# Optimization experiments

Measured on AMD Instinct MI355X. Metric: run time of the kernel, lower is better.

## Reference

```python
import jax, jax.numpy as jnp
import numpy as np

B_SZ, SEQ_LEN, STATE_DIM, D_IN, D_OUT, KX = 8, 2048, 1024, 512, 512, 10


def setup_inputs() -> dict:
    key = jax.random.key(0)
    ks = jax.random.split(key, 7)
    inputs = jax.random.normal(ks[0], (B_SZ, SEQ_LEN, D_IN), dtype=jnp.float32)
    h0 = jax.random.normal(ks[1], (STATE_DIM,), dtype=jnp.float32)
    # exponential_decay_init(lam=15): x = clamp(-1/lam * log(1-u), max=1); A = (1-x)*sign
    u = jax.random.uniform(ks[2], (STATE_DIM,), dtype=jnp.float32)
    x = jnp.minimum(-(1.0 / 15.0) * jnp.log1p(-u), 1.0)
    sign = jnp.sign(jax.random.normal(ks[3], (STATE_DIM,), dtype=jnp.float32))
    A = (1.0 - x) * sign
    Bm = jax.random.normal(ks[4], (D_IN, STATE_DIM), dtype=jnp.float32) / D_IN
    C = jax.random.normal(ks[5], (STATE_DIM, D_OUT), dtype=jnp.float32) / STATE_DIM
    M = jax.random.normal(ks[6], (D_OUT, D_IN, KX), dtype=jnp.float32) / D_OUT
    return {"inputs": inputs, "h0": h0, "A": A, "B": Bm, "C": C, "M": M}


def _ar_preds(M, x):
    # Equivalent to einsum('oik,bli->bklo') + per-k roll + triu mask + sum over k:
    # ar[b,l,:] = sum_{i=0}^{k-1, i<=l} M[:,:,i] @ x[b, l-i, :]
    b, l, d_in = x.shape
    kx = M.shape[2]
    ar = jnp.einsum('oi,bli->blo', M[:, :, 0], x)
    for i in range(1, kx):
        x_shift = jnp.pad(x, ((0, 0), (i, 0), (0, 0)))[:, :l]  # shift right, zero-fill
        ar = ar + jnp.einsum('oi,bli->blo', M[:, :, i], x_shift)
    return ar


def reference(inputs, h0, A, B, C, M):
    b, l, d_in = inputs.shape
    state_dim = A.shape[0]
    # Project inputs once: u_t @ B for all t -> [b, l, s]
    uB = jnp.einsum('bli,is->bls', inputs, B)

    def step(h, u_t):
        h = A * h + u_t  # diagonal recurrence
        return h, h

    h_init = jnp.broadcast_to(h0, (b, state_dim))
    _, hs = jax.lax.scan(step, h_init, jnp.swapaxes(uB, 0, 1))  # [l, b, s]
    hs = jnp.swapaxes(hs, 0, 1)  # [b, l, s]
    lds_out = hs @ C  # [b, l, d_out]
    return lds_out + _ar_preds(M, inputs)
```

## Files before the change

### kernel.cpp

```cpp
#include <hip/hip_runtime.h>

#define B_SZ   8
#define SEQ    2048
#define PSEQ   (SEQ+16)
#define SDIM   1024
#define DIN    512
#define DOUT   512
#define KX     10
#define RTOT   (B_SZ*SEQ)
#define LC     64
#define NC     (SEQ/LC)

typedef __attribute__((ext_vector_type(8))) short short8;
typedef __attribute__((ext_vector_type(4))) float f32x4;
typedef __attribute__((ext_vector_type(4))) unsigned short bfx4;

#define OFF_XP   0UL
#define OFF_UB   16973824UL
#define OFF_HS   50528256UL
#define OFF_BT   84082688UL
#define OFF_CT   85131264UL
#define OFF_MT   86179840UL

__device__ __forceinline__ short f2bf(float f) {
  unsigned u = __builtin_bit_cast(unsigned, f);
  u += 0x7fffu + ((u >> 16) & 1u);
  return (short)(u >> 16);
}
__device__ __forceinline__ float bf2f(unsigned short b) {
  return __builtin_bit_cast(float, (unsigned)b << 16);
}

#define GLOAD16(gp, lp) __builtin_amdgcn_global_load_lds( \
    (const __attribute__((address_space(1))) void*)(gp), \
    (__attribute__((address_space(3))) void*)(lp), 16, 0, 0)
#define WAITVM(n) asm volatile("s_waitcnt vmcnt(" #n ")" ::: "memory")
#define LGKM0()   do { asm volatile("s_waitcnt lgkmcnt(0)" ::: "memory"); \
                       __builtin_amdgcn_sched_barrier(0); } while (0)
#define SBAR() __builtin_amdgcn_s_barrier()

__device__ __forceinline__ void transpose_tile(const float* __restrict__ in,
                                               short* __restrict__ out,
                                               int rows, int cols, int bxi, int byi,
                                               int tid, float (*t)[33]) {
  int bx = bxi * 32, by = byi * 32;
  int tx = tid & 31, ty = tid >> 5;
  #pragma unroll
  for (int j = 0; j < 32; j += 8)
    t[ty + j][tx] = in[(size_t)(by + ty + j) * cols + (bx + tx)];
  __syncthreads();
  #pragma unroll
  for (int j = 0; j < 32; j += 8)
    out[(size_t)(bx + ty + j) * rows + (by + tx)] = f2bf(t[tx][ty + j]);
}

__global__ void k_prep(const float* __restrict__ x,  const float* __restrict__ B,
                       const float* __restrict__ C,  const float* __restrict__ M,
                       short* __restrict__ Xp, short* __restrict__ Bt,
                       short* __restrict__ Ct, short* __restrict__ Mt) {
  __shared__ float t[32][33];
  int blk = blockIdx.x, tid = threadIdx.x;
  if (blk < 2048) {
    const int NG = RTOT * (DIN / 8);
    const int NPAD = B_SZ * 16 * (DIN / 8);
    for (int g = blk * 256 + tid; g < NG + NPAD; g += 2048 * 256) {
      if (g < NG) {
        int r = g >> 6, c8 = g & 63;
        int b = r >> 11, tt = r & 2047;
        const float4* p = reinterpret_cast<const float4*>(x) + (size_t)g * 2;
        float4 f0 = p[0], f1 = p[1];
        short8 o;
        o[0]=f2bf(f0.x); o[1]=f2bf(f0.y); o[2]=f2bf(f0.z); o[3]=f2bf(f0.w);
        o[4]=f2bf(f1.x); o[5]=f2bf(f1.y); o[6]=f2bf(f1.z); o[7]=f2bf(f1.w);
        *reinterpret_cast<short8*>(Xp + ((size_t)(b * PSEQ + 16 + tt) * DIN + c8 * 8)) = o;
      } else {
        int idx = g - NG;
        int b = idx >> 10, rem = idx & 1023;
        int row16 = rem >> 6, c8 = rem & 63;
        const short8 z = {0,0,0,0,0,0,0,0};
        *reinterpret_cast<short8*>(Xp + ((size_t)(b * PSEQ + row16) * DIN + c8 * 8)) = z;
      }
    }
  } else if (blk < 2560) {
    int idx = blk - 2048;
    transpose_tile(B, Bt, DIN, SDIM, idx & 31, idx >> 5, tid, t);
  } else if (blk < 3072) {
    int idx = blk - 2560;
    transpose_tile(C, Ct, SDIM, DOUT, idx & 15, idx >> 4, tid, t);
  } else {
    int idx = (blk - 3072) * 256 + tid;
    if (idx < DOUT * DIN) {
      int o = idx / DIN, i = idx - o * DIN;
      const float* src = M + ((size_t)o * DIN + i) * KX;
      #pragma unroll
      for (int tt = 0; tt < KX; ++tt)
        Mt[((size_t)tt * DOUT + o) * DIN + i] = f2bf(src[tt]);
    }
  }
}

__global__ void k_scan_E(const short* __restrict__ uB, const float* __restrict__ A,
                         float* __restrict__ E) {
  int blk = blockIdx.x, tid = threadIdx.x;
  int b = blk >> 5, c = blk & 31;
  int s0 = tid * 4;
  const short* base = uB + ((size_t)b * SEQ + (size_t)c * LC) * SDIM + s0;
  float a[4], h[4];
  #pragma unroll
  for (int j = 0; j < 4; ++j) { a[j] = A[s0 + j]; h[j] = 0.f; }
  for (int t = 0; t < LC; ++t) {
    bfx4 v = *reinterpret_cast<const bfx4*>(base + (size_t)t * SDIM);
    #pragma unroll
    for (int j = 0; j < 4; ++j) h[j] = fmaf(a[j], h[j], bf2f(v[j]));
  }
  float* ep = E + (size_t)blk * SDIM + s0;
  #pragma unroll
  for (int j = 0; j < 4; ++j) ep[j] = h[j];
}

__global__ void k_scan_h(const short* __restrict__ uB, const float* __restrict__ A,
                         const float* __restrict__ h0, const float* __restrict__ E,
                         short* __restrict__ hs) {
  int blk = blockIdx.x, tid = threadIdx.x;
  int b = blk >> 5, c = blk & 31;
  int s0 = tid * 4;
  float a[4], h[4], ap[4];
  #pragma unroll
  for (int j = 0; j < 4; ++j) {
    a[j] = A[s0 + j];
    float p = a[j];
    #pragma unroll
    for (int q = 0; q < 6; ++q) p *= p;
    ap[j] = p;
    h[j] = h0[s0 + j];
  }
  const float* Eb = E + (size_t)b * NC * SDIM + s0;
  for (int c2 = 0; c2 < c; ++c2) {
    float4 ev = *reinterpret_cast<const float4*>(Eb + (size_t)c2 * SDIM);
    h[0] = fmaf(ap[0], h[0], ev.x);
    h[1] = fmaf(ap[1], h[1], ev.y);
    h[2] = fmaf(ap[2], h[2], ev.z);
    h[3] = fmaf(ap[3], h[3], ev.w);
  }
  const short* base = uB + ((size_t)b * SEQ + (size_t)c * LC) * SDIM + s0;
  short* hbase = hs + ((size_t)b * SEQ + (size_t)c * LC) * SDIM + s0;
  for (int t = 0; t < LC; ++t) {
    bfx4 v = *reinterpret_cast<const bfx4*>(base + (size_t)t * SDIM);
    bfx4 o;
    #pragma unroll
    for (int j = 0; j < 4; ++j) {
      h[j] = fmaf(a[j], h[j], bf2f(v[j]));
      o[j] = (unsigned short)f2bf(h[j]);
    }
    *reinterpret_cast<bfx4*>(hbase + (size_t)t * SDIM) = o;
  }
}

__device__ __forceinline__ void stage128(const short* __restrict__ g, int ld,
                                         short* l, int tid) {
  int rsub = tid >> 3;
  int slot = (tid & 7) ^ (rsub & 7);
  #pragma unroll
  for (int i = 0; i < 4; ++i) {
    int row = i * 32 + rsub;
    GLOAD16(g + (size_t)row * ld + slot * 8, l + row * 64 + (tid & 7) * 8);
  }
}

__device__ __forceinline__ void mfma_tile(const short* lA, int aoff, const short* lB,
                                          int lane, int wm, int wn, f32x4 acc[4][4]) {
  int lr = lane & 15;
  int h  = lane >> 4;
  #pragma unroll
  for (int kk = 0; kk < 2; ++kk) {
    int kslot = kk * 4 + h;
    short8 af[4], bfr[4];
    #pragma unroll
    for (int mi = 0; mi < 4; ++mi) {
      int row = aoff + wm * 64 + mi * 16 + lr;
      af[mi] = *reinterpret_cast<const short8*>(lA + row * 64 + ((kslot ^ (row & 7)) << 3));
    }
    #pragma unroll
    for (int ni = 0; ni < 4; ++ni) {
      int row = wn * 64 + ni * 16 + lr;
      bfr[ni] = *reinterpret_cast<const short8*>(lB + row * 64 + ((kslot ^ (row & 7)) << 3));
    }
    __builtin_amdgcn_s_setprio(1);
    #pragma unroll
    for (int mi = 0; mi < 4; ++mi)
      #pragma unroll
      for (int ni = 0; ni < 4; ++ni)
        acc[mi][ni] = __builtin_amdgcn_mfma_f32_16x16x32_bf16(af[mi], bfr[ni], acc[mi][ni], 0, 0, 0);
    __builtin_amdgcn_s_setprio(0);
  }
}

__global__ __launch_bounds__(256) void k_gemm_uB(const short* __restrict__ Xp,
                                                 const short* __restrict__ Bt,
                                                 short* __restrict__ uB) {
  __shared__ __attribute__((aligned(16))) short lds[32768];
  short* A0 = lds;         short* B0 = lds + 8192;
  short* A1 = lds + 16384; short* B1 = lds + 24576;
  int tid = threadIdx.x, lane = tid & 63, w = tid >> 6, wm = w >> 1, wn = w & 1;
  long r0 = (long)blockIdx.x * 128;
  int  c0 = blockIdx.y * 128;
  int  b  = (int)(r0 >> 11);
  const short* Abase = Xp + (size_t)(r0 + 16 * (b + 1)) * DIN;
  const short* Bbase = Bt + (size_t)c0 * DIN;
  const f32x4 z4 = {0.f, 0.f, 0.f, 0.f};
  f32x4 acc[4][4];
  #pragma unroll
  for (int mi = 0; mi < 4; ++mi)
    #pragma unroll
    for (int ni = 0; ni < 4; ++ni) acc[mi][ni] = z4;

  stage128(Abase, DIN, A0, tid);      stage128(Bbase, DIN, B0, tid);
  stage128(Abase + 64, DIN, A1, tid); stage128(Bbase + 64, DIN, B1, tid);
  WAITVM(8);
  SBAR();
  for (int kt = 0; kt < 8; ++kt) {
    const short* a  = (kt & 1) ? A1 : A0;
    const short* bb = (kt & 1) ? B1 : B0;
    mfma_tile(a, 0, bb, lane, wm, wn, acc);
    SBAR();
    if (kt + 2 < 8) {
      short* ad = (kt & 1) ? A1 : A0;
      short* bd = (kt & 1) ? B1 : B0;
      stage128(Abase + (kt + 2) * 64, DIN, ad, tid);
      stage128(Bbase + (kt + 2) * 64, DIN, bd, tid);
      WAITVM(8);
    } else {
      WAITVM(0);
    }
    SBAR();
  }
  #pragma unroll
  for (int mi = 0; mi < 4; ++mi)
    #pragma unroll
    for (int ni = 0; ni < 4; ++ni)
      #pragma unroll
      for (int r = 0; r < 4; ++r) {
        long row = r0 + wm * 64 + mi * 16 + (lane >> 4) * 4 + r;
        int  col = c0 + wn * 64 + ni * 16 + (lane & 15);
        uB[(size_t)row * SDIM + col] = f2bf(acc[mi][ni][r]);
      }
}

struct Frags { short8 a[4][2]; short8 b[4][2]; };

__device__ __forceinline__ void read_frags(Frags& f, const short* la, int aoff,
                                           const short* lb, int lane, int wm, int wn) {
  int lr = lane & 15, h = lane >> 4;
  #pragma unroll
  for (int kk = 0; kk < 2; ++kk) {
    int kslot = kk * 4 + h;
    #pragma unroll
    for (int mi = 0; mi < 4; ++mi) {
      int row = aoff + wm * 64 + mi * 16 + lr;
      f.a[mi][kk] = *reinterpret_cast<const short8*>(la + row * 64 + ((kslot ^ (row & 7)) << 3));
    }
    #pragma unroll
    for (int ni = 0; ni < 4; ++ni) {
      int row = wn * 64 + ni * 16 + lr;
      f.b[ni][kk] = *reinterpret_cast<const short8*>(lb + row * 64 + ((kslot ^ (row & 7)) << 3));
    }
  }
}

__device__ __forceinline__ void mfma_frags(const Frags& f, f32x4 acc[4][4]) {
  #pragma unroll
  for (int kk = 0; kk < 2; ++kk)
    #pragma unroll
    for (int mi = 0; mi < 4; ++mi)
      #pragma unroll
      for (int ni = 0; ni < 4; ++ni)
        acc[mi][ni] = __builtin_amdgcn_mfma_f32_16x16x32_bf16(f.a[mi][kk], f.b[ni][kk], acc[mi][ni], 0, 0, 0);
}

__device__ __forceinline__ void sgb_interleave() {
  #pragma unroll
  for (int i = 0; i < 16; ++i) {
    __builtin_amdgcn_sched_group_barrier(0x008, 2, 0);
    __builtin_amdgcn_sched_group_barrier(0x100, 1, 0);
  }
}

__device__ __forceinline__ void stageA256(const short* __restrict__ g, int ld,
                                          short* l, int tid) {
  int rsub = tid >> 3;
  int slot = (tid & 7) ^ (rsub & 7);
  #pragma unroll
  for (int i = 0; i < 4; ++i) {
    int row = i * 64 + rsub;
    GLOAD16(g + (size_t)row * ld + slot * 8, l + row * 64 + (tid & 7) * 8);
  }
}
__device__ __forceinline__ void stageB128(const short* __restrict__ g, int ld,
                                          short* l, int tid) {
  int rsub = tid >> 3;
  int slot = (tid & 7) ^ (rsub & 7);
  #pragma unroll
  for (int i = 0; i < 2; ++i) {
    int row = i * 64 + rsub;
    GLOAD16(g + (size_t)row * ld + slot * 8, l + row * 64 + (tid & 7) * 8);
  }
}
__device__ __forceinline__ void stageX320(const short* __restrict__ g,
                                          short* l, int tid) {
  int rsub = tid >> 3;
  int slot = (tid & 7) ^ (rsub & 7);
  #pragma unroll
  for (int i = 0; i < 5; ++i) {
    int row = i * 64 + rsub;
    GLOAD16(g + (size_t)row * DIN + slot * 8, l + row * 64 + (tid & 7) * 8);
  }
}

__global__ __launch_bounds__(512, 2) void k_gemm_out(const short* __restrict__ hs,
                                                     const short* __restrict__ Xp,
                                                     const short* __restrict__ Ct,
                                                     const short* __restrict__ Mt,
                                                     float* __restrict__ out) {
  __shared__ __attribute__((aligned(16))) short lds[81920];
  short* const P0  = lds;
  short* const P1  = lds + 24576;
  short* const P2  = lds + 49152;
  short* const Xs0 = lds;
  short* const Xs1 = lds + 20480;
  short* const PM0 = lds + 57344;
  short* const PM1 = lds + 65536;
  short* const PM2 = lds + 73728;
  int tid = threadIdx.x, lane = tid & 63, w = tid >> 6;
  int wm = w >> 1, wn = w & 1;
  int bid = blockIdx.x;
  int sw  = (bid & 7) * 32 + (bid >> 3);
  long r0 = (long)(sw & 63) * 256;
  int  c0 = (sw >> 6) * 128;
  int  b  = (int)(r0 >> 11);
  const short* hsA = hs + (size_t)r0 * SDIM;
  const short* CtB = Ct + (size_t)c0 * SDIM;
  const short* Xa  = Xp + (size_t)(r0 + 16 * (b + 1) - 16) * DIN;
  const short* MtB = Mt + (size_t)c0 * DIN;

  const f32x4 z4 = {0.f, 0.f, 0.f, 0.f};
  f32x4 acc[4][4];
  #pragma unroll
  for (int mi = 0; mi < 4; ++mi)
    #pragma unroll
    for (int ni = 0; ni < 4; ++ni) acc[mi][ni] = z4;

  Frags fr[2];

  stageA256(hsA,        SDIM, P0, tid);  stageB128(CtB,        SDIM, P0 + 16384, tid);
  stageA256(hsA + 64,   SDIM, P1, tid);  stageB128(CtB + 64,   SDIM, P1 + 16384, tid);
  stageA256(hsA + 128,  SDIM, P2, tid);  stageB128(CtB + 128,  SDIM, P2 + 16384, tid);
  WAITVM(6);
  SBAR();
  read_frags(fr[0], P0, 0, P0 + 16384, lane, wm, wn);

  #pragma unroll
  for (int s = 0; s < 16; ++s) {
    __builtin_amdgcn_s_setprio(1);
    mfma_frags(fr[s & 1], acc);
    if (s < 15) {
      const short* nb = ((s + 1) % 3 == 0) ? P0 : ((s + 1) % 3 == 1) ? P1 : P2;
      read_frags(fr[(s + 1) & 1], nb, 0, nb + 16384, lane, wm, wn);
    } else {
      read_frags(fr[0], Xs0, 16, PM0, lane, wm, wn);
    }
    sgb_interleave();
    __builtin_amdgcn_s_setprio(0);
    LGKM0();
    SBAR();
    if (s <= 12) {
      short* sp = (s % 3 == 0) ? P0 : (s % 3 == 1) ? P1 : P2;
      stageA256(hsA + (s + 3) * 64, SDIM, sp, tid);
      stageB128(CtB + (s + 3) * 64, SDIM, sp + 16384, tid);
      WAITVM(6);
    } else if (s == 13) {
      stageB128(MtB, DIN, PM0, tid);
      stageB128(MtB + (size_t)DOUT * DIN, DIN, PM1, tid);
      WAITVM(4);
    } else if (s == 14) {
      stageB128(MtB + (size_t)2 * DOUT * DIN, DIN, PM2, tid);
      stageX320(Xa, Xs0, tid);
      WAITVM(0);
    }
    SBAR();
  }

  for (int k0 = 0; k0 < 8; ++k0) {
    int kc = k0 * 64;
    const short* xs = (k0 & 1) ? Xs1 : Xs0;
    short*       xn = (k0 & 1) ? Xs0 : Xs1;
    const short* q0 = (k0 % 3 == 0) ? PM0 : (k0 % 3 == 1) ? PM1 : PM2;
    const short* q1 = (k0 % 3 == 0) ? PM1 : (k0 % 3 == 1) ? PM2 : PM0;
    const short* q2 = (k0 % 3 == 0) ? PM2 : (k0 % 3 == 1) ? PM0 : PM1;
    #pragma unroll
    for (int j = 0; j < KX; ++j) {
      __builtin_amdgcn_s_setprio(1);
      mfma_frags(fr[j & 1], acc);
      bool do_read = (j < 9) || (k0 < 7);
      if (j < 9) {
        const short* mn = ((j + 1) % 3 == 0) ? q0 : ((j + 1) % 3 == 1) ? q1 : q2;
        read_frags(fr[(j + 1) & 1], xs, 15 - j, mn, lane, wm, wn);
      } else if (k0 < 7) {
        read_frags(fr[0], xn, 16, q1, lane, wm, wn);
      }
      if (do_read) sgb_interleave();
      __builtin_amdgcn_s_setprio(0);
      LGKM0();
      SBAR();
      if (j + 3 <= 9) {
        short* mw = (j % 3 == 0) ? (short*)q0 : (j % 3 == 1) ? (short*)q1 : (short*)q2;
        stageB128(MtB + (size_t)(j + 3) * DOUT * DIN + kc, DIN, mw, tid);
      } else if (k0 < 7) {
        short* mw = (j % 3 == 0) ? (short*)q0 : (j % 3 == 1) ? (short*)q1 : (short*)q2;
        stageB128(MtB + (size_t)(j - 7) * DOUT * DIN + kc + 64, DIN, mw, tid);
      }
      if (j == 1 && k0 < 7) stageX320(Xa + kc + 64, xn, tid);
      if (j == 1 || j == 2) {
        if (k0 < 7) { WAITVM(7); } else { WAITVM(2); }
      } else if (j >= 7) {
        if (k0 == 7) { WAITVM(0); } else { WAITVM(2); }
      } else {
        WAITVM(2);
      }
      SBAR();
    }
  }

  #pragma unroll
  for (int mi = 0; mi < 4; ++mi)
    #pragma unroll
    for (int ni = 0; ni < 4; ++ni)
      #pragma unroll
      for (int r = 0; r < 4; ++r) {
        long row = r0 + wm * 64 + mi * 16 + (lane >> 4) * 4 + r;
        int  col = c0 + wn * 64 + ni * 16 + (lane & 15);
        out[(size_t)row * DOUT + col] = acc[mi][ni][r];
      }
}

extern "C" void kernel_launch(void* const* d_in, const int* in_sizes, int n_in,
                              void* d_out, int out_size, void* d_ws, size_t ws_size,
                              hipStream_t stream) {
  (void)in_sizes; (void)n_in; (void)out_size; (void)ws_size;
  const float* x  = (const float*)d_in[0];
  const float* h0 = (const float*)d_in[1];
  const float* A  = (const float*)d_in[2];
  const float* B  = (const float*)d_in[3];
  const float* C  = (const float*)d_in[4];
  const float* M  = (const float*)d_in[5];
  float* out = (float*)d_out;
  char* ws = (char*)d_ws;

  short* Xp  = (short*)(ws + OFF_XP);
  short* uB  = (short*)(ws + OFF_UB);
  short* hsb = (short*)(ws + OFF_HS);
  short* Bt  = (short*)(ws + OFF_BT);
  short* Ct  = (short*)(ws + OFF_CT);
  short* Mt  = (short*)(ws + OFF_MT);
  float* E   = out;

  k_prep<<<4096, 256, 0, stream>>>(x, B, C, M, Xp, Bt, Ct, Mt);
  k_gemm_uB<<<dim3(RTOT / 128, SDIM / 128), 256, 0, stream>>>(Xp, Bt, uB);
  k_scan_E<<<B_SZ * NC, 256, 0, stream>>>(uB, A, E);
  k_scan_h<<<B_SZ * NC, 256, 0, stream>>>(uB, A, h0, E, hsb);
  k_gemm_out<<<256, 512, 0, stream>>>(hsb, Xp, Ct, Mt, out);
}
```

Baseline: 151.8 us.

## Fuse chunk-end scan into uB GEMM epilogue and move C/M prep into scan kernel

The separate k_scan_E pass, which reread uB to compute each 64-step chunk's end state, is removed. The uB GEMM epilogue now computes that end state directly from its fp32 accumulators with powers of A and cross-lane shuffles. The C and M transpose/convert blocks move from the prep kernel into the k_scan_h launch so they run alongside the scan blocks. This saves one kernel launch and a full read of uB, at the cost of a heavier GEMM epilogue and a slight numeric difference, since E is now built from fp32 accumulators rather than bf16-rounded uB.

```diff
diff --git a/kernel.cpp b/kernel.cpp
--- a/kernel.cpp
+++ b/kernel.cpp
@@ -39,25 +39,8 @@
                        __builtin_amdgcn_sched_barrier(0); } while (0)
 #define SBAR() __builtin_amdgcn_s_barrier()
 
-__device__ __forceinline__ void transpose_tile(const float* __restrict__ in,
-                                               short* __restrict__ out,
-                                               int rows, int cols, int bxi, int byi,
-                                               int tid, float (*t)[33]) {
-  int bx = bxi * 32, by = byi * 32;
-  int tx = tid & 31, ty = tid >> 5;
-  #pragma unroll
-  for (int j = 0; j < 32; j += 8)
-    t[ty + j][tx] = in[(size_t)(by + ty + j) * cols + (bx + tx)];
-  __syncthreads();
-  #pragma unroll
-  for (int j = 0; j < 32; j += 8)
-    out[(size_t)(bx + ty + j) * rows + (by + tx)] = f2bf(t[tx][ty + j]);
-}
-
-__global__ void k_prep(const float* __restrict__ x,  const float* __restrict__ B,
-                       const float* __restrict__ C,  const float* __restrict__ M,
-                       short* __restrict__ Xp, short* __restrict__ Bt,
-                       short* __restrict__ Ct, short* __restrict__ Mt) {
+__global__ void k_prep1(const float* __restrict__ x, const float* __restrict__ B,
+                        short* __restrict__ Xp, short* __restrict__ Bt) {
   __shared__ float t[32][33];
   int blk = blockIdx.x, tid = threadIdx.x;
   if (blk < 2048) {
@@ -81,14 +64,73 @@
         *reinterpret_cast<short8*>(Xp + ((size_t)(b * PSEQ + row16) * DIN + c8 * 8)) = z;
       }
     }
-  } else if (blk < 2560) {
+  } else {
     int idx = blk - 2048;
-    transpose_tile(B, Bt, DIN, SDIM, idx & 31, idx >> 5, tid, t);
-  } else if (blk < 3072) {
-    int idx = blk - 2560;
-    transpose_tile(C, Ct, SDIM, DOUT, idx & 15, idx >> 4, tid, t);
+    int bx = (idx & 31) * 32, by = (idx >> 5) * 32;
+    int tx = tid & 31, ty = tid >> 5;
+    #pragma unroll
+    for (int j = 0; j < 32; j += 8)
+      t[ty + j][tx] = B[(size_t)(by + ty + j) * SDIM + (bx + tx)];
+    __syncthreads();
+    #pragma unroll
+    for (int j = 0; j < 32; j += 8)
+      Bt[(size_t)(bx + ty + j) * DIN + (by + tx)] = f2bf(t[tx][ty + j]);
+  }
+}
+
+__global__ void k_scan_h(const short* __restrict__ uB, const float* __restrict__ A,
+                         const float* __restrict__ h0, const float* __restrict__ E,
+                         short* __restrict__ hs,
+                         const float* __restrict__ C, const float* __restrict__ M,
+                         short* __restrict__ Ct, short* __restrict__ Mt) {
+  __shared__ float t[32][33];
+  int blk = blockIdx.x, tid = threadIdx.x;
+  if (blk < 256) {
+    int b = blk >> 5, c = blk & 31;
+    int s0 = tid * 4;
+    float a[4], h[4], ap[4];
+    #pragma unroll
+    for (int j = 0; j < 4; ++j) {
+      a[j] = A[s0 + j];
+      float p = a[j];
+      #pragma unroll
+      for (int q = 0; q < 6; ++q) p *= p;
+      ap[j] = p;
+      h[j] = h0[s0 + j];
+    }
+    const float* Eb = E + (size_t)b * NC * SDIM + s0;
+    for (int c2 = 0; c2 < c; ++c2) {
+      float4 ev = *reinterpret_cast<const float4*>(Eb + (size_t)c2 * SDIM);
+      h[0] = fmaf(ap[0], h[0], ev.x);
+      h[1] = fmaf(ap[1], h[1], ev.y);
+      h[2] = fmaf(ap[2], h[2], ev.z);
+      h[3] = fmaf(ap[3], h[3], ev.w);
+    }
+    const short* base = uB + ((size_t)b * SEQ + (size_t)c * LC) * SDIM + s0;
+    short* hbase = hs + ((size_t)b * SEQ + (size_t)c * LC) * SDIM + s0;
+    for (int tt = 0; tt < LC; ++tt) {
+      bfx4 v = *reinterpret_cast<const bfx4*>(base + (size_t)tt * SDIM);
+      bfx4 o;
+      #pragma unroll
+      for (int j = 0; j < 4; ++j) {
+        h[j] = fmaf(a[j], h[j], bf2f(v[j]));
+        o[j] = (unsigned short)f2bf(h[j]);
+      }
+      *reinterpret_cast<bfx4*>(hbase + (size_t)tt * SDIM) = o;
+    }
+  } else if (blk < 768) {
+    int idx = blk - 256;
+    int bx = (idx & 15) * 32, by = (idx >> 4) * 32;
+    int tx = tid & 31, ty = tid >> 5;
+    #pragma unroll
+    for (int j = 0; j < 32; j += 8)
+      t[ty + j][tx] = C[(size_t)(by + ty + j) * DOUT + (bx + tx)];
+    __syncthreads();
+    #pragma unroll
+    for (int j = 0; j < 32; j += 8)
+      Ct[(size_t)(bx + ty + j) * SDIM + (by + tx)] = f2bf(t[tx][ty + j]);
   } else {
-    int idx = (blk - 3072) * 256 + tid;
+    int idx = (blk - 768) * 256 + tid;
     if (idx < DOUT * DIN) {
       int o = idx / DIN, i = idx - o * DIN;
       const float* src = M + ((size_t)o * DIN + i) * KX;
@@ -96,63 +138,6 @@
       for (int tt = 0; tt < KX; ++tt)
         Mt[((size_t)tt * DOUT + o) * DIN + i] = f2bf(src[tt]);
     }
-  }
-}
-
-__global__ void k_scan_E(const short* __restrict__ uB, const float* __restrict__ A,
-                         float* __restrict__ E) {
-  int blk = blockIdx.x, tid = threadIdx.x;
-  int b = blk >> 5, c = blk & 31;
-  int s0 = tid * 4;
-  const short* base = uB + ((size_t)b * SEQ + (size_t)c * LC) * SDIM + s0;
-  float a[4], h[4];
-  #pragma unroll
-  for (int j = 0; j < 4; ++j) { a[j] = A[s0 + j]; h[j] = 0.f; }
-  for (int t = 0; t < LC; ++t) {
-    bfx4 v = *reinterpret_cast<const bfx4*>(base + (size_t)t * SDIM);
-    #pragma unroll
-    for (int j = 0; j < 4; ++j) h[j] = fmaf(a[j], h[j], bf2f(v[j]));
-  }
-  float* ep = E + (size_t)blk * SDIM + s0;
-  #pragma unroll
-  for (int j = 0; j < 4; ++j) ep[j] = h[j];
-}
-
-__global__ void k_scan_h(const short* __restrict__ uB, const float* __restrict__ A,
-                         const float* __restrict__ h0, const float* __restrict__ E,
-                         short* __restrict__ hs) {
-  int blk = blockIdx.x, tid = threadIdx.x;
-  int b = blk >> 5, c = blk & 31;
-  int s0 = tid * 4;
-  float a[4], h[4], ap[4];
-  #pragma unroll
-  for (int j = 0; j < 4; ++j) {
-    a[j] = A[s0 + j];
-    float p = a[j];
-    #pragma unroll
-    for (int q = 0; q < 6; ++q) p *= p;
-    ap[j] = p;
-    h[j] = h0[s0 + j];
-  }
-  const float* Eb = E + (size_t)b * NC * SDIM + s0;
-  for (int c2 = 0; c2 < c; ++c2) {
-    float4 ev = *reinterpret_cast<const float4*>(Eb + (size_t)c2 * SDIM);
-    h[0] = fmaf(ap[0], h[0], ev.x);
-    h[1] = fmaf(ap[1], h[1], ev.y);
-    h[2] = fmaf(ap[2], h[2], ev.z);
-    h[3] = fmaf(ap[3], h[3], ev.w);
-  }
-  const short* base = uB + ((size_t)b * SEQ + (size_t)c * LC) * SDIM + s0;
-  short* hbase = hs + ((size_t)b * SEQ + (size_t)c * LC) * SDIM + s0;
-  for (int t = 0; t < LC; ++t) {
-    bfx4 v = *reinterpret_cast<const bfx4*>(base + (size_t)t * SDIM);
-    bfx4 o;
-    #pragma unroll
-    for (int j = 0; j < 4; ++j) {
-      h[j] = fmaf(a[j], h[j], bf2f(v[j]));
-      o[j] = (unsigned short)f2bf(h[j]);
-    }
-    *reinterpret_cast<bfx4*>(hbase + (size_t)t * SDIM) = o;
   }
 }
 
@@ -197,7 +182,9 @@
 
 __global__ __launch_bounds__(256) void k_gemm_uB(const short* __restrict__ Xp,
                                                  const short* __restrict__ Bt,
-                                                 short* __restrict__ uB) {
+                                                 short* __restrict__ uB,
+                                                 const float* __restrict__ Adecay,
+                                                 float* __restrict__ E) {
   __shared__ __attribute__((aligned(16))) short lds[32768];
   short* A0 = lds;         short* B0 = lds + 8192;
   short* A1 = lds + 16384; short* B1 = lds + 24576;
@@ -234,16 +221,37 @@
     }
     SBAR();
   }
+  int h = lane >> 4;
   #pragma unroll
   for (int mi = 0; mi < 4; ++mi)
     #pragma unroll
     for (int ni = 0; ni < 4; ++ni)
       #pragma unroll
       for (int r = 0; r < 4; ++r) {
-        long row = r0 + wm * 64 + mi * 16 + (lane >> 4) * 4 + r;
+        long row = r0 + wm * 64 + mi * 16 + h * 4 + r;
         int  col = c0 + wn * 64 + ni * 16 + (lane & 15);
         uB[(size_t)row * SDIM + col] = f2bf(acc[mi][ni][r]);
       }
+  int cch = (int)((r0 >> 6) & 31) + wm;
+  #pragma unroll
+  for (int ni = 0; ni < 4; ++ni) {
+    int col = c0 + wn * 64 + ni * 16 + (lane & 15);
+    float a  = Adecay[col];
+    float a2 = a * a, a3 = a2 * a;
+    float A4 = a2 * a2;
+    float A16 = A4 * A4; A16 = A16 * A16;
+    float P16_2 = A16 * A16, P16_3 = P16_2 * A16;
+    float Q4 = (h == 3) ? 1.f : (h == 2) ? A4 : (h == 1) ? A4 * A4 : A4 * A4 * A4;
+    float cm0 = fmaf(acc[0][ni][0], a3, fmaf(acc[0][ni][1], a2, fmaf(acc[0][ni][2], a, acc[0][ni][3])));
+    float cm1 = fmaf(acc[1][ni][0], a3, fmaf(acc[1][ni][1], a2, fmaf(acc[1][ni][2], a, acc[1][ni][3])));
+    float cm2 = fmaf(acc[2][ni][0], a3, fmaf(acc[2][ni][1], a2, fmaf(acc[2][ni][2], a, acc[2][ni][3])));
+    float cm3 = fmaf(acc[3][ni][0], a3, fmaf(acc[3][ni][1], a2, fmaf(acc[3][ni][2], a, acc[3][ni][3])));
+    float L = fmaf(cm0, P16_3, fmaf(cm1, P16_2, fmaf(cm2, A16, cm3)));
+    L *= Q4;
+    L += __shfl_xor(L, 16);
+    L += __shfl_xor(L, 32);
+    if (h == 0) E[((size_t)b * NC + cch) * SDIM + col] = L;
+  }
 }
 
 struct Frags { short8 a[4][2]; short8 b[4][2]; };
@@ -463,9 +471,8 @@
   short* Mt  = (short*)(ws + OFF_MT);
   float* E   = out;
 
-  k_prep<<<4096, 256, 0, stream>>>(x, B, C, M, Xp, Bt, Ct, Mt);
-  k_gemm_uB<<<dim3(RTOT / 128, SDIM / 128), 256, 0, stream>>>(Xp, Bt, uB);
-  k_scan_E<<<B_SZ * NC, 256, 0, stream>>>(uB, A, E);
-  k_scan_h<<<B_SZ * NC, 256, 0, stream>>>(uB, A, h0, E, hsb);
+  k_prep1<<<2560, 256, 0, stream>>>(x, B, Xp, Bt);
+  k_gemm_uB<<<dim3(RTOT / 128, SDIM / 128), 256, 0, stream>>>(Xp, Bt, uB, A, E);
+  k_scan_h<<<1792, 256, 0, stream>>>(uB, A, h0, E, hsb, C, M, Ct, Mt);
   k_gemm_out<<<256, 512, 0, stream>>>(hsb, Xp, Ct, Mt, out);
 }
```

Result: faster. 147.0 us (-3.1%).
